# Kernel tuning notes

Measured on AMD Instinct MI355X. Metric: run time of the kernel, lower is better.

## Reference

```python
import jax, jax.numpy as jnp
import numpy as np

VOCAB = 50257
H = 512  # output_size == embed dim == lstm hidden
N = 65536  # number of tokens


def setup_inputs() -> dict:
    key = jax.random.key(0)
    ks = jax.random.split(key, 12)
    s = 1.0 / np.sqrt(H)  # torch LSTM/Linear init scale
    inp = {
        "ids": jax.random.randint(ks[0], (N,), 0, VOCAB, dtype=jnp.int64)
        if jax.config.jax_enable_x64 else jax.random.randint(ks[0], (N,), 0, VOCAB, dtype=jnp.int32),
        "emb": jax.random.normal(ks[1], (VOCAB, H), dtype=jnp.float32),
        # LSTM layer 0 (gate order: i, f, g, o)
        "W_ih0": jax.random.uniform(ks[2], (4 * H, H), jnp.float32, -s, s),
        "W_hh0": jax.random.uniform(ks[3], (4 * H, H), jnp.float32, -s, s),
        "b_ih0": jax.random.uniform(ks[4], (4 * H,), jnp.float32, -s, s),
        "b_hh0": jax.random.uniform(ks[5], (4 * H,), jnp.float32, -s, s),
        # LSTM layer 1
        "W_ih1": jax.random.uniform(ks[6], (4 * H, H), jnp.float32, -s, s),
        "W_hh1": jax.random.uniform(ks[7], (4 * H, H), jnp.float32, -s, s),
        "b_ih1": jax.random.uniform(ks[8], (4 * H,), jnp.float32, -s, s),
        "b_hh1": jax.random.uniform(ks[9], (4 * H,), jnp.float32, -s, s),
        # final Linear
        "W_lin": jax.random.uniform(ks[10], (H, H), jnp.float32, -s, s),
        "b_lin": jax.random.uniform(ks[11], (H,), jnp.float32, -s, s),
    }
    return inp


def _lstm_cell_zero_state(x, W_ih, b_ih, b_hh):
    # Single LSTM step with h_prev = c_prev = 0, so W_hh @ h_prev == 0.
    # gates: [N, 4H] in torch order i, f, g, o
    gates = x @ W_ih.T + (b_ih + b_hh)
    i, f, g, o = jnp.split(gates, 4, axis=-1)
    c = jax.nn.sigmoid(i) * jnp.tanh(g)  # f * c_prev == 0
    h = jax.nn.sigmoid(o) * jnp.tanh(c)
    return h


def reference(ids, emb, W_ih0, W_hh0, b_ih0, b_hh0, W_ih1, W_hh1, b_ih1, b_hh1, W_lin, b_lin):
    # Each token is processed with a fresh zero LSTM state, so the python
    # loop in the original vectorizes exactly over the token dim.
    x = emb[ids]                                   # [N, H]
    h0 = _lstm_cell_zero_state(x, W_ih0, b_ih0, b_hh0)   # layer 1 hidden
    h1 = _lstm_cell_zero_state(h0, W_ih1, b_ih1, b_hh1)  # layer 2 hidden (hidden[-1])
    out = jax.nn.relu(h1 @ W_lin.T + b_lin)        # [N, H]
    return out[:, None, :]                         # stacked [N, 1, H] like torch.stack of [1,H]
```

## Files before the change

kernel.cpp:

```cpp
#include <hip/hip_runtime.h>
#include <stdint.h>


typedef _Float16 half8 __attribute__((ext_vector_type(8)));
typedef __attribute__((ext_vector_type(4))) float float4v;
typedef __attribute__((ext_vector_type(4))) unsigned int uint4v;

__device__ __forceinline__ float sigmoidf_(float x) { return 1.0f / (1.0f + __expf(-x)); }
__device__ __forceinline__ float tanhf_(float x) { return 1.0f - 2.0f / (__expf(2.0f * x) + 1.0f); }

__device__ __forceinline__ void gl2lds16(const void* g, void* l) {
  __builtin_amdgcn_global_load_lds(
      (const __attribute__((address_space(1))) void*)g,
      (__attribute__((address_space(3))) void*)l, 16, 0, 0);
}

__global__ __launch_bounds__(256) void prep_kernel(
    const float* __restrict__ emb,
    const float* __restrict__ W0, const float* __restrict__ bi0, const float* __restrict__ bh0,
    const float* __restrict__ W1, const float* __restrict__ bi1, const float* __restrict__ bh1,
    const float* __restrict__ WL,
    _Float16* __restrict__ Ef,
    _Float16* __restrict__ W0f, _Float16* __restrict__ W1f, _Float16* __restrict__ WLf,
    float* __restrict__ b0p, float* __restrict__ b1p)
{
  int id = blockIdx.x * 256 + threadIdx.x;
  if (id < 3216448) {
    const float* s = emb + (size_t)id * 8;
    float4v v0 = *(const float4v*)s;
    float4v v1 = *(const float4v*)(s + 4);
    union { _Float16 h[8]; uint4v u; } P;
#pragma unroll
    for (int e = 0; e < 4; ++e) { P.h[e] = (_Float16)v0[e]; P.h[4 + e] = (_Float16)v1[e]; }
    *(uint4v*)(Ef + (size_t)id * 8) = P.u;
  } else if (id < 3347520) {
    int u = id - 3216448;
    int np = u >> 6, k0 = (u & 63) << 3;
    int n = ((np & 3) << 9) | (np >> 2);
    const float* s = W0 + n * 512 + k0;
    float4v v0 = *(const float4v*)s;
    float4v v1 = *(const float4v*)(s + 4);
    union { _Float16 h[8]; uint4v u; } P;
#pragma unroll
    for (int e = 0; e < 4; ++e) { P.h[e] = (_Float16)v0[e]; P.h[4 + e] = (_Float16)v1[e]; }
    *(uint4v*)(W0f + np * 512 + k0) = P.u;
  } else if (id < 3478592) {
    int u = id - 3347520;
    int np = u >> 6, k0 = (u & 63) << 3;
    int n = ((np & 3) << 9) | (np >> 2);
    const float* s = W1 + n * 512 + k0;
    float4v v0 = *(const float4v*)s;
    float4v v1 = *(const float4v*)(s + 4);
    union { _Float16 h[8]; uint4v u; } P;
#pragma unroll
    for (int e = 0; e < 4; ++e) { P.h[e] = (_Float16)v0[e]; P.h[4 + e] = (_Float16)v1[e]; }
    *(uint4v*)(W1f + np * 512 + k0) = P.u;
  } else if (id < 3511360) {
    int u = id - 3478592;
    const float* s = WL + (size_t)u * 8;
    float4v v0 = *(const float4v*)s;
    float4v v1 = *(const float4v*)(s + 4);
    union { _Float16 h[8]; uint4v u8; } P;
#pragma unroll
    for (int e = 0; e < 4; ++e) { P.h[e] = (_Float16)v0[e]; P.h[4 + e] = (_Float16)v1[e]; }
    *(uint4v*)(WLf + (size_t)u * 8) = P.u8;
  } else if (id < 3513408) {
    int np = id - 3511360;
    int n = ((np & 3) << 9) | (np >> 2);
    b0p[np] = bi0[n] + bh0[n];
  } else if (id < 3515456) {
    int np = id - 3513408;
    int n = ((np & 3) << 9) | (np >> 2);
    b1p[np] = bi1[n] + bh1[n];
  }
}

template <int MODE>
__global__ __launch_bounds__(512, 4) void gemm_kernel(
    const _Float16* __restrict__ A, const int* __restrict__ ids,
    const _Float16* __restrict__ B, const float* __restrict__ bias,
    _Float16* __restrict__ Of, float* __restrict__ Out,
    int nbShift, int nbMask)
{
  __shared__ __align__(16) char smem[36864];
  _Float16* sA = (_Float16*)smem;
  _Float16* sB = (_Float16*)(smem + 16384);

  const int T = threadIdx.x;
  const int lane = T & 63;
  const int wv = T >> 6;
  const int wrow = wv >> 1, wcol = wv & 1;
  const int mb = (int)blockIdx.x >> nbShift;
  const int nb = (int)blockIdx.x & nbMask;
  const size_t t0 = (size_t)mb * 256;
  const int n0 = nb * 128;

  const int r0 = T >> 2;
  const int qg = (T & 3) ^ ((r0 >> 1) & 3);
  size_t sr0 = t0 + r0, sr1 = t0 + 128 + r0;
  if (ids) { sr0 = (size_t)(unsigned)ids[sr0]; sr1 = (size_t)(unsigned)ids[sr1]; }
  const _Float16* gA0 = A + sr0 * 512 + qg * 8;
  const _Float16* gA1 = A + sr1 * 512 + qg * 8;
  const _Float16* gB  = B + (size_t)(n0 + r0) * 512 + qg * 8;

  const int m_ = lane & 15, qf = lane >> 4;
  const int qs = qf ^ ((m_ >> 1) & 3);
  const int offA = wrow * 2048 + m_ * 32 + qs * 8;
  const int offB = wcol * 2048 + m_ * 32 + qs * 8;

  float4v acc[4][4];
#pragma unroll
  for (int i = 0; i < 4; ++i)
#pragma unroll
    for (int j = 0; j < 4; ++j)
      acc[i][j] = (float4v){0.f, 0.f, 0.f, 0.f};

  for (int it = 0; it < 16; ++it) {
    gl2lds16(gA0, sA + T * 8);
    gl2lds16(gA1, sA + 4096 + T * 8);
    gl2lds16(gB,  sB + T * 8);
    gA0 += 32; gA1 += 32; gB += 32;
    __syncthreads();

    half8 a[4], b[4];
#pragma unroll
    for (int i = 0; i < 4; ++i) {
      a[i] = *(const half8*)(sA + offA + i * 512);
      b[i] = *(const half8*)(sB + offB + i * 512);
    }
#pragma unroll
    for (int i = 0; i < 4; ++i)
#pragma unroll
      for (int j = 0; j < 4; ++j)
        acc[i][j] = __builtin_amdgcn_mfma_f32_16x16x32_f16(b[j], a[i], acc[i][j], 0, 0, 0);
    __syncthreads();
  }

  float4v bq[4];
#pragma unroll
  for (int j = 0; j < 4; ++j)
    bq[j] = *(const float4v*)(bias + n0 + wcol * 64 + j * 16 + qf * 4);

  if (MODE == 0) {
    float* hT = (float*)smem;
#pragma unroll
    for (int i = 0; i < 4; ++i) {
      const int trow = wrow * 64 + i * 16 + m_;
#pragma unroll
      for (int j = 0; j < 4; ++j) {
        float yi = acc[i][j][0] + bq[j][0];
        float yg = acc[i][j][2] + bq[j][2];
        float yo = acc[i][j][3] + bq[j][3];
        float cc = sigmoidf_(yi) * tanhf_(yg);
        float hh = sigmoidf_(yo) * tanhf_(cc);
        hT[trow * 36 + wcol * 16 + j * 4 + qf] = hh;
      }
    }
    __syncthreads();
    const int tl = T >> 1, hf = T & 1;
    const float* src = hT + tl * 36 + hf * 16;
    float4v r0 = *(const float4v*)(src);
    float4v r1 = *(const float4v*)(src + 4);
    float4v r2 = *(const float4v*)(src + 8);
    float4v r3 = *(const float4v*)(src + 12);
    union { _Float16 h[8]; uint4v v; } P0, P1;
#pragma unroll
    for (int e = 0; e < 4; ++e) {
      P0.h[e] = (_Float16)r0[e]; P0.h[4 + e] = (_Float16)r1[e];
      P1.h[e] = (_Float16)r2[e]; P1.h[4 + e] = (_Float16)r3[e];
    }
    _Float16* dst = Of + (t0 + tl) * 512 + (size_t)(nb * 32) + hf * 16;
    *(uint4v*)dst = P0.v;
    *(uint4v*)(dst + 8) = P1.v;
  } else {
#pragma unroll
    for (int i = 0; i < 4; ++i) {
      const size_t row = t0 + wrow * 64 + i * 16 + m_;
#pragma unroll
      for (int j = 0; j < 4; ++j) {
        float4v v;
#pragma unroll
        for (int r = 0; r < 4; ++r)
          v[r] = fmaxf(acc[i][j][r] + bq[j][r], 0.0f);
        *(float4v*)(Out + row * 512 + (size_t)(n0 + wcol * 64 + j * 16 + qf * 4)) = v;
      }
    }
  }
}

extern "C" void kernel_launch(void* const* d_in, const int* in_sizes, int n_in,
                              void* d_out, int out_size, void* d_ws, size_t ws_size,
                              hipStream_t stream) {
  (void)in_sizes; (void)n_in; (void)out_size; (void)ws_size;
  const int*   ids   = (const int*)d_in[0];
  const float* emb   = (const float*)d_in[1];
  const float* W0    = (const float*)d_in[2];
  const float* bi0   = (const float*)d_in[4];
  const float* bh0   = (const float*)d_in[5];
  const float* W1    = (const float*)d_in[6];
  const float* bi1   = (const float*)d_in[8];
  const float* bh1   = (const float*)d_in[9];
  const float* WL    = (const float*)d_in[10];
  const float* blin  = (const float*)d_in[11];
  float* out = (float*)d_out;

  char* ws = (char*)d_ws;
  const size_t MB = 1024 * 1024;
  _Float16* W0f = (_Float16*)(ws);
  _Float16* W1f = (_Float16*)(ws + 2 * MB);
  _Float16* WLf = (_Float16*)(ws + 4 * MB);
  float*    b0p = (float*)(ws + 4 * MB + 512 * 1024);
  float*    b1p = (float*)(ws + 4 * MB + 512 * 1024 + 8192);
  _Float16* Ef  = (_Float16*)(ws + 8 * MB);
  _Float16* H1f = Ef;
  _Float16* H0f = (_Float16*)(ws + 72 * MB);

  prep_kernel<<<13733, 256, 0, stream>>>(emb, W0, bi0, bh0, W1, bi1, bh1, WL,
                                         Ef, W0f, W1f, WLf, b0p, b1p);
  gemm_kernel<0><<<4096, 512, 0, stream>>>(Ef, ids, W0f, b0p, H0f, nullptr, 4, 15);
  gemm_kernel<0><<<4096, 512, 0, stream>>>(H0f, nullptr, W1f, b1p, H1f, nullptr, 4, 15);
  gemm_kernel<1><<<1024, 512, 0, stream>>>(H1f, nullptr, WLf, blin, nullptr, out, 2, 3);
}
```

Before: 661.3 us.

## Double-buffer LDS tiles and enlarge per-wave tile in GEMM kernels

Each GEMM block now runs with 256 threads instead of 512, and each wave computes a 128x64 sub-tile (8x4 MFMA accumulators) instead of 64x64. Global-to-LDS loads for the next K-slice are issued into a second LDS buffer while the current slice is being computed, with explicit vmcnt waits, which hides load latency behind MFMA work. Block indices are swizzled across groups of 8 to improve cache locality. The epilogue stages fp16 instead of fp32 in LDS. The larger accumulator set and double buffer raise register and LDS use, which may lower occupancy.

```diff
diff --git a/kernel.cpp b/kernel.cpp
--- a/kernel.cpp
+++ b/kernel.cpp
@@ -76,64 +76,103 @@
 }
 
 template <int MODE>
-__global__ __launch_bounds__(512, 4) void gemm_kernel(
+__global__ __launch_bounds__(256, 2) void gemm_kernel(
     const _Float16* __restrict__ A, const int* __restrict__ ids,
     const _Float16* __restrict__ B, const float* __restrict__ bias,
     _Float16* __restrict__ Of, float* __restrict__ Out,
     int nbShift, int nbMask)
 {
-  __shared__ __align__(16) char smem[36864];
-  _Float16* sA = (_Float16*)smem;
-  _Float16* sB = (_Float16*)(smem + 16384);
-
+  __shared__ __align__(16) char smem[49152];
   const int T = threadIdx.x;
   const int lane = T & 63;
   const int wv = T >> 6;
   const int wrow = wv >> 1, wcol = wv & 1;
-  const int mb = (int)blockIdx.x >> nbShift;
-  const int nb = (int)blockIdx.x & nbMask;
+
+  const int nwg = (int)gridDim.x;
+  const int bid = (int)blockIdx.x;
+  const int swz = (bid & 7) * (nwg >> 3) + (bid >> 3);
+  const int mb = swz >> nbShift;
+  const int nb = swz & nbMask;
   const size_t t0 = (size_t)mb * 256;
   const int n0 = nb * 128;
 
   const int r0 = T >> 2;
   const int qg = (T & 3) ^ ((r0 >> 1) & 3);
-  size_t sr0 = t0 + r0, sr1 = t0 + 128 + r0;
-  if (ids) { sr0 = (size_t)(unsigned)ids[sr0]; sr1 = (size_t)(unsigned)ids[sr1]; }
-  const _Float16* gA0 = A + sr0 * 512 + qg * 8;
-  const _Float16* gA1 = A + sr1 * 512 + qg * 8;
-  const _Float16* gB  = B + (size_t)(n0 + r0) * 512 + qg * 8;
+  size_t ra0 = t0 + r0, ra1 = t0 + 64 + r0, ra2 = t0 + 128 + r0, ra3 = t0 + 192 + r0;
+  if (ids) {
+    ra0 = (size_t)(unsigned)ids[ra0]; ra1 = (size_t)(unsigned)ids[ra1];
+    ra2 = (size_t)(unsigned)ids[ra2]; ra3 = (size_t)(unsigned)ids[ra3];
+  }
+  const _Float16* gA0 = A + ra0 * 512 + qg * 8;
+  const _Float16* gA1 = A + ra1 * 512 + qg * 8;
+  const _Float16* gA2 = A + ra2 * 512 + qg * 8;
+  const _Float16* gA3 = A + ra3 * 512 + qg * 8;
+  const _Float16* gB0 = B + (size_t)(n0 + r0) * 512 + qg * 8;
+  const _Float16* gB1 = B + (size_t)(n0 + 64 + r0) * 512 + qg * 8;
 
   const int m_ = lane & 15, qf = lane >> 4;
   const int qs = qf ^ ((m_ >> 1) & 3);
-  const int offA = wrow * 2048 + m_ * 32 + qs * 8;
-  const int offB = wcol * 2048 + m_ * 32 + qs * 8;
-
-  float4v acc[4][4];
-#pragma unroll
-  for (int i = 0; i < 4; ++i)
+  const int offA = (wrow * 128 + m_) * 32 + qs * 8;
+  const int offB = (wcol * 64 + m_) * 32 + qs * 8;
+
+  float4v acc[8][4];
+#pragma unroll
+  for (int i = 0; i < 8; ++i)
 #pragma unroll
     for (int j = 0; j < 4; ++j)
       acc[i][j] = (float4v){0.f, 0.f, 0.f, 0.f};
 
+  _Float16* sA0 = (_Float16*)smem;
+  _Float16* sB0 = (_Float16*)(smem + 16384);
+  _Float16* sA1 = (_Float16*)(smem + 24576);
+  _Float16* sB1 = (_Float16*)(smem + 40960);
+
+  gl2lds16(gA0, sA0 + T * 8);
+  gl2lds16(gA1, sA0 + 2048 + T * 8);
+  gl2lds16(gA2, sA0 + 4096 + T * 8);
+  gl2lds16(gA3, sA0 + 6144 + T * 8);
+  gl2lds16(gB0, sB0 + T * 8);
+  gl2lds16(gB1, sB0 + 2048 + T * 8);
+  gA0 += 32; gA1 += 32; gA2 += 32; gA3 += 32; gB0 += 32; gB1 += 32;
+
+  const _Float16* sAc = sA0;
+  const _Float16* sBc = sB0;
+  _Float16* sAn = sA1;
+  _Float16* sBn = sB1;
+
+#pragma unroll 2
   for (int it = 0; it < 16; ++it) {
-    gl2lds16(gA0, sA + T * 8);
-    gl2lds16(gA1, sA + 4096 + T * 8);
-    gl2lds16(gB,  sB + T * 8);
-    gA0 += 32; gA1 += 32; gB += 32;
-    __syncthreads();
-
-    half8 a[4], b[4];
-#pragma unroll
-    for (int i = 0; i < 4; ++i) {
-      a[i] = *(const half8*)(sA + offA + i * 512);
-      b[i] = *(const half8*)(sB + offB + i * 512);
+    if (it < 15) {
+      gl2lds16(gA0, sAn + T * 8);
+      gl2lds16(gA1, sAn + 2048 + T * 8);
+      gl2lds16(gA2, sAn + 4096 + T * 8);
+      gl2lds16(gA3, sAn + 6144 + T * 8);
+      gl2lds16(gB0, sBn + T * 8);
+      gl2lds16(gB1, sBn + 2048 + T * 8);
+      gA0 += 32; gA1 += 32; gA2 += 32; gA3 += 32; gB0 += 32; gB1 += 32;
+      asm volatile("s_waitcnt vmcnt(6)" ::: "memory");
+    } else {
+      asm volatile("s_waitcnt vmcnt(0)" ::: "memory");
     }
-#pragma unroll
-    for (int i = 0; i < 4; ++i)
+    __builtin_amdgcn_sched_barrier(0);
+    __builtin_amdgcn_s_barrier();
+
+    half8 a[8], b[4];
+#pragma unroll
+    for (int i = 0; i < 8; ++i) a[i] = *(const half8*)(sAc + offA + i * 512);
+#pragma unroll
+    for (int j = 0; j < 4; ++j) b[j] = *(const half8*)(sBc + offB + j * 512);
+#pragma unroll
+    for (int i = 0; i < 8; ++i)
 #pragma unroll
       for (int j = 0; j < 4; ++j)
         acc[i][j] = __builtin_amdgcn_mfma_f32_16x16x32_f16(b[j], a[i], acc[i][j], 0, 0, 0);
-    __syncthreads();
+
+    asm volatile("s_waitcnt lgkmcnt(0)" ::: "memory");
+    __builtin_amdgcn_sched_barrier(0);
+    __builtin_amdgcn_s_barrier();
+    const _Float16* tA = sAc; sAc = sAn; sAn = (_Float16*)tA;
+    const _Float16* tB = sBc; sBc = sBn; sBn = (_Float16*)tB;
   }
 
   float4v bq[4];
@@ -142,10 +181,11 @@
     bq[j] = *(const float4v*)(bias + n0 + wcol * 64 + j * 16 + qf * 4);
 
   if (MODE == 0) {
-    float* hT = (float*)smem;
-#pragma unroll
-    for (int i = 0; i < 4; ++i) {
-      const int trow = wrow * 64 + i * 16 + m_;
+    _Float16* hT = (_Float16*)smem;
+    const int u0 = wcol * 16 + qf;
+#pragma unroll
+    for (int i = 0; i < 8; ++i) {
+      const int trow = wrow * 128 + i * 16 + m_;
 #pragma unroll
       for (int j = 0; j < 4; ++j) {
         float yi = acc[i][j][0] + bq[j][0];
@@ -153,29 +193,24 @@
         float yo = acc[i][j][3] + bq[j][3];
         float cc = sigmoidf_(yi) * tanhf_(yg);
         float hh = sigmoidf_(yo) * tanhf_(cc);
-        hT[trow * 36 + wcol * 16 + j * 4 + qf] = hh;
+        hT[trow * 40 + u0 + j * 4] = (_Float16)hh;
       }
     }
     __syncthreads();
-    const int tl = T >> 1, hf = T & 1;
-    const float* src = hT + tl * 36 + hf * 16;
-    float4v r0 = *(const float4v*)(src);
-    float4v r1 = *(const float4v*)(src + 4);
-    float4v r2 = *(const float4v*)(src + 8);
-    float4v r3 = *(const float4v*)(src + 12);
-    union { _Float16 h[8]; uint4v v; } P0, P1;
-#pragma unroll
-    for (int e = 0; e < 4; ++e) {
-      P0.h[e] = (_Float16)r0[e]; P0.h[4 + e] = (_Float16)r1[e];
-      P1.h[e] = (_Float16)r2[e]; P1.h[4 + e] = (_Float16)r3[e];
-    }
-    _Float16* dst = Of + (t0 + tl) * 512 + (size_t)(nb * 32) + hf * 16;
-    *(uint4v*)dst = P0.v;
-    *(uint4v*)(dst + 8) = P1.v;
+    const _Float16* src = hT + T * 40;
+    uint4v v0 = *(const uint4v*)(src);
+    uint4v v1 = *(const uint4v*)(src + 8);
+    uint4v v2 = *(const uint4v*)(src + 16);
+    uint4v v3 = *(const uint4v*)(src + 24);
+    _Float16* dst = Of + (t0 + T) * 512 + (size_t)(nb * 32);
+    *(uint4v*)(dst) = v0;
+    *(uint4v*)(dst + 8) = v1;
+    *(uint4v*)(dst + 16) = v2;
+    *(uint4v*)(dst + 24) = v3;
   } else {
 #pragma unroll
-    for (int i = 0; i < 4; ++i) {
-      const size_t row = t0 + wrow * 64 + i * 16 + m_;
+    for (int i = 0; i < 8; ++i) {
+      const size_t row = t0 + wrow * 128 + i * 16 + m_;
 #pragma unroll
       for (int j = 0; j < 4; ++j) {
         float4v v;
@@ -217,7 +252,7 @@
 
   prep_kernel<<<13733, 256, 0, stream>>>(emb, W0, bi0, bh0, W1, bi1, bh1, WL,
                                          Ef, W0f, W1f, WLf, b0p, b1p);
-  gemm_kernel<0><<<4096, 512, 0, stream>>>(Ef, ids, W0f, b0p, H0f, nullptr, 4, 15);
-  gemm_kernel<0><<<4096, 512, 0, stream>>>(H0f, nullptr, W1f, b1p, H1f, nullptr, 4, 15);
-  gemm_kernel<1><<<1024, 512, 0, stream>>>(H1f, nullptr, WLf, blin, nullptr, out, 2, 3);
-}
+  gemm_kernel<0><<<4096, 256, 0, stream>>>(Ef, ids, W0f, b0p, H0f, nullptr, 4, 15);
+  gemm_kernel<0><<<4096, 256, 0, stream>>>(H0f, nullptr, W1f, b1p, H1f, nullptr, 4, 15);
+  gemm_kernel<1><<<1024, 256, 0, stream>>>(H1f, nullptr, WLf, blin, nullptr, out, 2, 3);
+}
```

Result: faster. 648.2 us (-2.0%).
